# Kernel tuning notes

Measured on AMD Instinct MI355X. Metric: run time of the kernel, lower is better.

The kernel has to match this reference:

```python
import jax, jax.numpy as jnp
import numpy as np

S, B, SD, OD = 10, 256, 16, 8
H = 10 * (SD * SD + OD * OD)        # 3200, gru hidden
OUT1 = 4 * SD * OD                  # 512
IN = 2 * (SD + OD)                  # 48
TEMP = 0.1                          # concrete-dropout temperature


def setup_inputs() -> dict:
    key = jax.random.key(0)
    ks = jax.random.split(key, 24)
    sc = lambda k, sh, s=0.05: jax.random.normal(k, sh, jnp.float32) * s
    return {
        "y_t": sc(ks[0], (B, OD), 1.0),
        "x_filtered_prev": sc(ks[1], (B, SD), 1.0),
        "x_filtered_prev_prev": sc(ks[2], (B, SD), 1.0),
        "y_prev": sc(ks[3], (B, OD), 1.0),
        "delta_x_prev": sc(ks[4], (B, SD), 1.0),
        "h_prev_ensemble": sc(ks[5], (S, B, H)),
        "F_mat": sc(ks[6], (SD, SD), 0.2),
        "H_mat": sc(ks[7], (OD, SD), 0.2),
        "fc_in_w": sc(ks[8], (H, IN)),
        "fc_in_b": jnp.zeros((H,), jnp.float32),
        "W_ih": sc(ks[9], (3 * H, H), 0.01),
        "W_hh": sc(ks[10], (3 * H, H), 0.01),
        "b_ih": jnp.zeros((3 * H,), jnp.float32),
        "b_hh": jnp.zeros((3 * H,), jnp.float32),
        "fc1_w": sc(ks[11], (OUT1, H)),
        "fc1_b": jnp.zeros((OUT1,), jnp.float32),
        "fc2_w": sc(ks[12], (SD * OD, OUT1)),
        "fc2_b": jnp.zeros((SD * OD,), jnp.float32),
        "p_logit1": jnp.array([0.5], jnp.float32),   # sigmoid -> p in (0.5, 0.8) range
        "p_logit2": jnp.array([1.0], jnp.float32),
        "u1": jax.random.uniform(ks[13], (S, B, H), jnp.float32, 1e-4, 1.0 - 1e-4),
        "u2": jax.random.uniform(ks[14], (S, B, OUT1), jnp.float32, 1e-4, 1.0 - 1e-4),
    }


def _concrete_dropout(x, u, p):
    # relaxed Bernoulli drop mask, scaled to keep expectation
    z = jax.nn.sigmoid((jnp.log(p) - jnp.log1p(-p) + jnp.log(u) - jnp.log1p(-u)) / TEMP)
    return x * (1.0 - z) / (1.0 - p)


def reference(y_t, x_filtered_prev, x_filtered_prev_prev, y_prev, delta_x_prev,
              h_prev_ensemble, F_mat, H_mat, fc_in_w, fc_in_b,
              W_ih, W_hh, b_ih, b_hh, fc1_w, fc1_b, fc2_w, fc2_b,
              p_logit1, p_logit2, u1, u2):
    # system model prediction (nonlinear f, linear h), vectorized over batch
    x_predicted = jnp.tanh(x_filtered_prev @ F_mat.T)          # (B, SD)
    y_predicted = x_predicted @ H_mat.T                        # (B, OD)

    residual = y_t - y_predicted
    diff_state = x_filtered_prev - x_filtered_prev_prev
    inp = jnp.concatenate([delta_x_prev, residual, diff_state, y_prev], axis=-1)  # (B, IN)
    a = jax.nn.relu(inp @ fc_in_w.T + fc_in_b)                 # (B, H) shared across ensemble

    p1 = jax.nn.sigmoid(p_logit1[0])
    p2 = jax.nn.sigmoid(p_logit2[0])

    def gru_cell(x, h):
        gx = x @ W_ih.T + b_ih
        gh = h @ W_hh.T + b_hh
        gx_r, gx_z, gx_n = jnp.split(gx, 3, axis=-1)
        gh_r, gh_z, gh_n = jnp.split(gh, 3, axis=-1)
        r = jax.nn.sigmoid(gx_r + gh_r)
        z = jax.nn.sigmoid(gx_z + gh_z)
        n = jnp.tanh(gx_n + r * gh_n)
        return (1.0 - z) * n + z * h

    def sample_fn(h_i, u1_i, u2_i):
        x = _concrete_dropout(a, u1_i, p1)                     # (B, H)
        h_new = gru_cell(x, h_i)                               # (B, H)
        o = jax.nn.relu(h_new @ fc1_w.T + fc1_b)               # (B, OUT1)
        o = _concrete_dropout(o, u2_i, p2)
        K = (o @ fc2_w.T + fc2_b).reshape(B, SD, OD)           # Kalman gain
        correction = jnp.einsum('bso,bo->bs', K, residual)
        return x_predicted + correction, h_new

    xf_ens, h_new_ens = jax.vmap(sample_fn)(h_prev_ensemble, u1, u2)  # (S,B,SD),(S,B,H)

    x_filtered_final = xf_ens.mean(axis=0)                     # (B, SD)
    diff = xf_ens - x_filtered_final                           # (S, B, SD)
    P_filtered_final = jnp.einsum('sbi,sbj->bij', diff, diff) / S

    # concrete-dropout regularizer (identical per ensemble member)
    ent = lambda p: p * jnp.log(p) + (1.0 - p) * jnp.log1p(-p)
    reg = (jnp.sum(fc_in_w ** 2) / (1.0 - p1) + H * ent(p1)
           + jnp.sum(fc1_w ** 2) / (1.0 - p2) + OUT1 * ent(p2))
    raw_regularization = jnp.full((S,), reg)

    return x_filtered_final, P_filtered_final, raw_regularization
```

## Files before the change

kernel.cpp:

```cpp
#include <hip/hip_runtime.h>
#include <hip/hip_bf16.h>
#include <math.h>

#define S_ENS 10
#define B_DIM 256
#define SD 16
#define OD 8
#define H_DIM 3200
#define OUT1 512
#define IN_DIM 48
#define M_ROWS (S_ENS * B_DIM)
#define TEMP_INV 10.0f

typedef unsigned short u16;
typedef __attribute__((ext_vector_type(8))) short short8;
typedef __attribute__((ext_vector_type(4))) short short4v;
typedef __attribute__((ext_vector_type(4))) float floatx4;

__device__ __forceinline__ float sigmoidf_(float x) { return 1.0f / (1.0f + __expf(-x)); }
__device__ __forceinline__ float fast_tanh(float x) {
    x = fminf(fmaxf(x, -15.f), 15.f);
    float e = __expf(2.f * x);
    return (e - 1.f) / (e + 1.f);
}

__device__ __forceinline__ u16 f2bf(float f) {
    union { float f; unsigned u; } v; v.f = f;
    unsigned u = v.u + 0x7fffu + ((v.u >> 16) & 1u);
    return (u16)(u >> 16);
}
__device__ __forceinline__ float bf2f(u16 h) {
    union { unsigned u; float f; } v; v.u = ((unsigned)h) << 16;
    return v.f;
}

__device__ __forceinline__ void gld_lds16(const u16* g, u16* l) {
    __builtin_amdgcn_global_load_lds((const __attribute__((address_space(1))) void*)g,
                                     (__attribute__((address_space(3))) void*)l, 16, 0, 0);
}

__device__ __forceinline__ void kloop128(const u16* __restrict__ A, const u16* __restrict__ B,
                                         int m_base, int n_base, int kiters,
                                         u16* sA, u16* sB, floatx4 (&acc)[4][4]) {
    const int tid = threadIdx.x;
    const int wave = tid >> 6, lane = tid & 63;
    const int r = tid >> 2, c = tid & 3;
    const int swe = (c ^ ((r >> 1) & 3)) << 3;
    const u16* Ag = A + (size_t)(m_base + r) * H_DIM + swe;
    const u16* Bg = B + (size_t)(n_base + r) * H_DIM + swe;
    u16* sA0 = sA + wave * 512;
    u16* sB0 = sB + wave * 512;
    const int frow = lane & 15, fch = lane >> 4;
    const int wrow0 = (wave >> 1) * 64, wcol0 = (wave & 1) * 64;
    int aoff[4], boff[4];
    #pragma unroll
    for (int mi = 0; mi < 4; ++mi) {
        int row = wrow0 + mi * 16 + frow;
        aoff[mi] = row * 32 + ((fch ^ ((row >> 1) & 3)) << 3);
    }
    #pragma unroll
    for (int ni = 0; ni < 4; ++ni) {
        int row = wcol0 + ni * 16 + frow;
        boff[ni] = row * 32 + ((fch ^ ((row >> 1) & 3)) << 3);
    }
    for (int kk = 0; kk < kiters; ++kk) {
        const u16* ga = Ag + kk * 32;
        const u16* gb = Bg + kk * 32;
        __syncthreads();
        gld_lds16(ga, sA0);
        gld_lds16(ga + (size_t)64 * H_DIM, sA0 + 2048);
        gld_lds16(gb, sB0);
        gld_lds16(gb + (size_t)64 * H_DIM, sB0 + 2048);
        __syncthreads();
        short8 af[4], bfr[4];
        #pragma unroll
        for (int mi = 0; mi < 4; ++mi) af[mi] = *(const short8*)(sA + aoff[mi]);
        #pragma unroll
        for (int ni = 0; ni < 4; ++ni) bfr[ni] = *(const short8*)(sB + boff[ni]);
        #pragma unroll
        for (int mi = 0; mi < 4; ++mi)
            #pragma unroll
            for (int ni = 0; ni < 4; ++ni)
                acc[mi][ni] = __builtin_amdgcn_mfma_f32_16x16x32_bf16(af[mi], bfr[ni], acc[mi][ni], 0, 0, 0);
    }
}

__global__ __launch_bounds__(256) void gru_gemm_a(
    const u16* __restrict__ Xbf, const u16* __restrict__ Hpbf,
    const u16* __restrict__ Wih, const u16* __restrict__ Whh,
    const float* __restrict__ b_ih, const float* __restrict__ b_hh,
    u16* __restrict__ Rb, u16* __restrict__ Zb, u16* __restrict__ Gb) {
    __shared__ u16 sA[4096], sB[4096];
    floatx4 acc[4][4];
    #pragma unroll
    for (int i = 0; i < 4; ++i)
        #pragma unroll
        for (int j = 0; j < 4; ++j) acc[i][j] = (floatx4){0.f, 0.f, 0.f, 0.f};
    const int g = blockIdx.z;
    const int bmi = blockIdx.x, nbi = blockIdx.y;
    const int m_base = bmi * 128, nb = nbi * 128;
    const size_t gstride = (size_t)H_DIM * H_DIM;
    u16* outp;
    if (g == 0) {
        kloop128(Xbf, Wih, m_base, nb, 100, sA, sB, acc);
        kloop128(Hpbf, Whh, m_base, nb, 100, sA, sB, acc);
        outp = Rb;
    } else if (g == 1) {
        kloop128(Xbf, Wih + gstride, m_base, nb, 100, sA, sB, acc);
        kloop128(Hpbf, Whh + gstride, m_base, nb, 100, sA, sB, acc);
        outp = Zb;
    } else {
        kloop128(Hpbf, Whh + 2 * gstride, m_base, nb, 100, sA, sB, acc);
        outp = Gb;
    }
    const int lane = threadIdx.x & 63, wave = threadIdx.x >> 6;
    const int wcol0 = (wave & 1) * 64, cc = lane & 15;
    const size_t tbase = (size_t)(nbi * 20 + bmi) * 16384 + wave * 4096 + lane * 4;
    #pragma unroll
    for (int ni = 0; ni < 4; ++ni) {
        int col = nb + wcol0 + ni * 16 + cc;
        float bsum;
        if (g == 0)      bsum = b_ih[col] + b_hh[col];
        else if (g == 1) bsum = b_ih[H_DIM + col] + b_hh[H_DIM + col];
        else             bsum = b_hh[2 * H_DIM + col];
        #pragma unroll
        for (int mi = 0; mi < 4; ++mi) {
            short4v o;
            #pragma unroll
            for (int j = 0; j < 4; ++j) {
                float v = acc[mi][ni][j] + bsum;
                if (g < 2) v = sigmoidf_(v);
                o[j] = (short)f2bf(v);
            }
            *(short4v*)(outp + tbase + (mi * 4 + ni) * 256) = o;
        }
    }
}

__global__ __launch_bounds__(256) void gru_gemm_b(
    const u16* __restrict__ Xbf, const u16* __restrict__ Wih,
    const u16* __restrict__ Rb, const u16* __restrict__ Zb, const u16* __restrict__ Gb,
    const float* __restrict__ b_ih,
    const float* __restrict__ hprev, u16* __restrict__ Hn) {
    __shared__ u16 sA[4096], sB[4096];
    floatx4 acc[4][4];
    #pragma unroll
    for (int i = 0; i < 4; ++i)
        #pragma unroll
        for (int j = 0; j < 4; ++j) acc[i][j] = (floatx4){0.f, 0.f, 0.f, 0.f};
    const int bmi = blockIdx.x, nbi = blockIdx.y;
    const int m_base = bmi * 128, nb = nbi * 128;
    kloop128(Xbf, Wih + (size_t)2 * H_DIM * H_DIM, m_base, nb, 100, sA, sB, acc);
    const int lane = threadIdx.x & 63, wave = threadIdx.x >> 6;
    const int wrow0 = (wave >> 1) * 64, wcol0 = (wave & 1) * 64;
    const int quad = lane >> 4, cc = lane & 15;
    const size_t tbase = (size_t)(nbi * 20 + bmi) * 16384 + wave * 4096 + lane * 4;
    #pragma unroll
    for (int ni = 0; ni < 4; ++ni) {
        int col = nb + wcol0 + ni * 16 + cc;
        float bin_ = b_ih[2 * H_DIM + col];
        #pragma unroll
        for (int mi = 0; mi < 4; ++mi) {
            size_t pidx = tbase + (mi * 4 + ni) * 256;
            short4v rv = *(const short4v*)(Rb + pidx);
            short4v zv = *(const short4v*)(Zb + pidx);
            short4v gv = *(const short4v*)(Gb + pidx);
            int rw = m_base + wrow0 + mi * 16 + quad * 4;
            #pragma unroll
            for (int j = 0; j < 4; ++j) {
                float r = bf2f((u16)rv[j]);
                float z = bf2f((u16)zv[j]);
                float gh = bf2f((u16)gv[j]);
                float n = fast_tanh(acc[mi][ni][j] + bin_ + r * gh);
                size_t idx = (size_t)(rw + j) * H_DIM + col;
                float h = hprev[idx];
                Hn[idx] = f2bf((1.f - z) * n + z * h);
            }
        }
    }
}

__global__ __launch_bounds__(256) void fc1_k(
    const u16* __restrict__ Hn, const u16* __restrict__ Wb,
    const float* __restrict__ bias, const float* __restrict__ u2,
    const float* __restrict__ pl2, float* __restrict__ O) {
    __shared__ u16 sA[4096], sB[2048];
    floatx4 acc[4][2];
    #pragma unroll
    for (int i = 0; i < 4; ++i) { acc[i][0] = (floatx4){0.f,0.f,0.f,0.f}; acc[i][1] = (floatx4){0.f,0.f,0.f,0.f}; }
    const int tid = threadIdx.x;
    const int wave = tid >> 6, lane = tid & 63;
    const int m_base = blockIdx.y * 128, nb = blockIdx.x * 64;
    const int r = tid >> 2, c = tid & 3;
    const int swe = (c ^ ((r >> 1) & 3)) << 3;
    const u16* Ag = Hn + (size_t)(m_base + r) * H_DIM + swe;
    const u16* Bg = Wb + (size_t)(nb + r) * H_DIM + swe;
    u16* sA0 = sA + wave * 512;
    u16* sB0 = sB + wave * 512;
    const int frow = lane & 15, fch = lane >> 4;
    const int wrow0 = (wave >> 1) * 64, wcol0 = (wave & 1) * 32;
    int aoff[4], boff[2];
    #pragma unroll
    for (int mi = 0; mi < 4; ++mi) {
        int row = wrow0 + mi * 16 + frow;
        aoff[mi] = row * 32 + ((fch ^ ((row >> 1) & 3)) << 3);
    }
    #pragma unroll
    for (int ni = 0; ni < 2; ++ni) {
        int row = wcol0 + ni * 16 + frow;
        boff[ni] = row * 32 + ((fch ^ ((row >> 1) & 3)) << 3);
    }
    for (int kk = 0; kk < 100; ++kk) {
        __syncthreads();
        gld_lds16(Ag + kk * 32, sA0);
        gld_lds16(Ag + kk * 32 + (size_t)64 * H_DIM, sA0 + 2048);
        gld_lds16(Bg + kk * 32, sB0);
        __syncthreads();
        short8 af[4], bfr[2];
        #pragma unroll
        for (int mi = 0; mi < 4; ++mi) af[mi] = *(const short8*)(sA + aoff[mi]);
        #pragma unroll
        for (int ni = 0; ni < 2; ++ni) bfr[ni] = *(const short8*)(sB + boff[ni]);
        #pragma unroll
        for (int mi = 0; mi < 4; ++mi)
            #pragma unroll
            for (int ni = 0; ni < 2; ++ni)
                acc[mi][ni] = __builtin_amdgcn_mfma_f32_16x16x32_bf16(af[mi], bfr[ni], acc[mi][ni], 0, 0, 0);
    }
    float p = sigmoidf_(pl2[0]);
    float lp = __logf(p) - log1pf(-p);
    float inv = 1.0f / (1.0f - p);
    const int quad = lane >> 4, cc = lane & 15;
    #pragma unroll
    for (int ni = 0; ni < 2; ++ni) {
        int col = nb + wcol0 + ni * 16 + cc;
        float bcol = bias[col];
        #pragma unroll
        for (int mi = 0; mi < 4; ++mi) {
            int rw = m_base + wrow0 + mi * 16 + quad * 4;
            #pragma unroll
            for (int j = 0; j < 4; ++j) {
                size_t idx = (size_t)(rw + j) * OUT1 + col;
                float v = fmaxf(acc[mi][ni][j] + bcol, 0.f);
                float u = u2[idx];
                float z = sigmoidf_((lp + __logf(u) - log1pf(-u)) * TEMP_INV);
                O[idx] = v * (1.0f - z) * inv;
            }
        }
    }
}

__global__ void cvt_bf16_k(const float* __restrict__ src, u16* __restrict__ dst, int n8) {
    int i = blockIdx.x * 256 + threadIdx.x;
    if (i >= n8) return;
    float4 v0 = *((const float4*)src + 2 * (size_t)i);
    float4 v1 = *((const float4*)src + 2 * (size_t)i + 1);
    short8 o;
    o[0] = (short)f2bf(v0.x); o[1] = (short)f2bf(v0.y);
    o[2] = (short)f2bf(v0.z); o[3] = (short)f2bf(v0.w);
    o[4] = (short)f2bf(v1.x); o[5] = (short)f2bf(v1.y);
    o[6] = (short)f2bf(v1.z); o[7] = (short)f2bf(v1.w);
    *(short8*)(dst + 8 * (size_t)i) = o;
}

__global__ void prep_k(const float* __restrict__ y_t, const float* __restrict__ xfp,
                       const float* __restrict__ xfpp, const float* __restrict__ yprev,
                       const float* __restrict__ dxp, const float* __restrict__ Fm,
                       const float* __restrict__ Hm,
                       float* __restrict__ xpred, float* __restrict__ resid,
                       float* __restrict__ inp) {
    int b = threadIdx.x;
    float xrow[SD], xp[SD];
    for (int k = 0; k < SD; ++k) xrow[k] = xfp[b * SD + k];
    for (int s = 0; s < SD; ++s) {
        float acc = 0.f;
        for (int k = 0; k < SD; ++k) acc += xrow[k] * Fm[s * SD + k];
        xp[s] = tanhf(acc);
        xpred[b * SD + s] = xp[s];
    }
    float res[OD];
    for (int o = 0; o < OD; ++o) {
        float acc = 0.f;
        for (int s = 0; s < SD; ++s) acc += xp[s] * Hm[o * SD + s];
        res[o] = y_t[b * OD + o] - acc;
        resid[b * OD + o] = res[o];
    }
    float* ir = inp + b * IN_DIM;
    for (int k = 0; k < SD; ++k) ir[k] = dxp[b * SD + k];
    for (int o = 0; o < OD; ++o) ir[SD + o] = res[o];
    for (int k = 0; k < SD; ++k) ir[SD + OD + k] = xrow[k] - xfpp[b * SD + k];
    for (int o = 0; o < OD; ++o) ir[SD + OD + SD + o] = yprev[b * OD + o];
}

__global__ void fc_in_k(const float* __restrict__ inp, const float* __restrict__ w,
                        const float* __restrict__ bias, float* __restrict__ a) {
    int b = blockIdx.x;
    __shared__ float row[IN_DIM];
    int t = threadIdx.x;
    if (t < IN_DIM) row[t] = inp[b * IN_DIM + t];
    __syncthreads();
    for (int j = t; j < H_DIM; j += 256) {
        float s = bias[j];
        const float* wr = w + j * IN_DIM;
        #pragma unroll 8
        for (int k = 0; k < IN_DIM; ++k) s += row[k] * wr[k];
        a[b * H_DIM + j] = fmaxf(s, 0.f);
    }
}

__global__ void dropx_k(const float* __restrict__ a, const float* __restrict__ u1,
                        const float* __restrict__ pl1, u16* __restrict__ X) {
    int idx_in = blockIdx.x * 256 + threadIdx.x;
    int i = blockIdx.y;
    float p = sigmoidf_(pl1[0]);
    float lp = __logf(p) - log1pf(-p);
    float inv = 1.0f / (1.0f - p);
    size_t gidx = (size_t)i * (B_DIM * H_DIM) + idx_in;
    float u = u1[gidx];
    float z = sigmoidf_((lp + __logf(u) - log1pf(-u)) * TEMP_INV);
    X[gidx] = f2bf(a[idx_in] * (1.0f - z) * inv);
}

__global__ void fc2_corr_k(const float* __restrict__ O, const float* __restrict__ w,
                           const float* __restrict__ bias, const float* __restrict__ resid,
                           const float* __restrict__ xpred, float* __restrict__ xf_ens) {
    int row = blockIdx.x;
    int b = row & (B_DIM - 1);
    __shared__ __align__(16) float orow[OUT1];
    int t = threadIdx.x;
    for (int k = t; k < OUT1; k += 128) orow[k] = O[(size_t)row * OUT1 + k];
    __syncthreads();
    int s = t >> 3, oo = t & 7;
    const float* wr = w + (s * OD + oo) * OUT1;
    float sum = 0.f;
    for (int k = 0; k < OUT1; k += 4) {
        float4 ov = *(const float4*)&orow[k];
        float4 wv = *(const float4*)&wr[k];
        sum += ov.x * wv.x + ov.y * wv.y + ov.z * wv.z + ov.w * wv.w;
    }
    sum += bias[s * OD + oo];
    float v = sum * resid[b * OD + oo];
    v += __shfl_down(v, 4, 8);
    v += __shfl_down(v, 2, 8);
    v += __shfl_down(v, 1, 8);
    if (oo == 0) xf_ens[row * SD + s] = xpred[b * SD + s] + v;
}

__global__ void stats_k(const float* __restrict__ xf_ens, float* __restrict__ out) {
    int b = blockIdx.x;
    __shared__ float xf[S_ENS][SD];
    __shared__ float mean[SD];
    int t = threadIdx.x;
    if (t < S_ENS * SD) {
        int s = t >> 4, k = t & 15;
        xf[s][k] = xf_ens[s * (B_DIM * SD) + b * SD + k];
    }
    __syncthreads();
    if (t < SD) {
        float m = 0.f;
        for (int s = 0; s < S_ENS; ++s) m += xf[s][t];
        m *= (1.0f / S_ENS);
        mean[t] = m;
        out[b * SD + t] = m;
    }
    __syncthreads();
    int i = t >> 4, j = t & 15;
    float p = 0.f;
    for (int s = 0; s < S_ENS; ++s) p += (xf[s][i] - mean[i]) * (xf[s][j] - mean[j]);
    out[B_DIM * SD + b * 256 + t] = p * (1.0f / S_ENS);
}

__global__ void sumsq_k(const float* __restrict__ w, int n, float* __restrict__ accum) {
    float s = 0.f;
    for (int i = blockIdx.x * blockDim.x + threadIdx.x; i < n; i += gridDim.x * blockDim.x) {
        float v = w[i];
        s += v * v;
    }
    #pragma unroll
    for (int d = 32; d >= 1; d >>= 1) s += __shfl_down(s, d, 64);
    __shared__ float red[4];
    int lane = threadIdx.x & 63, wv = threadIdx.x >> 6;
    if (lane == 0) red[wv] = s;
    __syncthreads();
    if (threadIdx.x == 0) atomicAdd(accum, red[0] + red[1] + red[2] + red[3]);
}

__global__ void write_reg_k(const float* __restrict__ sums, const float* __restrict__ pl1,
                            const float* __restrict__ pl2, float* __restrict__ out) {
    int t = threadIdx.x;
    float p1 = sigmoidf_(pl1[0]);
    float p2 = sigmoidf_(pl2[0]);
    float ent1 = p1 * logf(p1) + (1.f - p1) * log1pf(-p1);
    float ent2 = p2 * logf(p2) + (1.f - p2) * log1pf(-p2);
    float reg = sums[0] / (1.f - p1) + (float)H_DIM * ent1
              + sums[1] / (1.f - p2) + (float)OUT1 * ent2;
    if (t < S_ENS) out[B_DIM * SD + B_DIM * SD * SD + t] = reg;
}

extern "C" void kernel_launch(void* const* d_in, const int* in_sizes, int n_in,
                              void* d_out, int out_size, void* d_ws, size_t ws_size,
                              hipStream_t stream) {
    const float* y_t     = (const float*)d_in[0];
    const float* xfp     = (const float*)d_in[1];
    const float* xfpp    = (const float*)d_in[2];
    const float* yprev   = (const float*)d_in[3];
    const float* dxp     = (const float*)d_in[4];
    const float* hprev   = (const float*)d_in[5];
    const float* Fm      = (const float*)d_in[6];
    const float* Hm      = (const float*)d_in[7];
    const float* fc_in_w = (const float*)d_in[8];
    const float* fc_in_b = (const float*)d_in[9];
    const float* W_ih    = (const float*)d_in[10];
    const float* W_hh    = (const float*)d_in[11];
    const float* b_ih    = (const float*)d_in[12];
    const float* b_hh    = (const float*)d_in[13];
    const float* fc1_w   = (const float*)d_in[14];
    const float* fc1_b   = (const float*)d_in[15];
    const float* fc2_w   = (const float*)d_in[16];
    const float* fc2_b   = (const float*)d_in[17];
    const float* pl1     = (const float*)d_in[18];
    const float* pl2     = (const float*)d_in[19];
    const float* u1      = (const float*)d_in[20];
    const float* u2      = (const float*)d_in[21];
    float* out = (float*)d_out;
    char* ws = (char*)d_ws;

    const size_t SZ_W    = (size_t)3 * H_DIM * H_DIM * 2;
    const size_t SZ_MH   = (size_t)M_ROWS * H_DIM * 2;
    size_t off = 0;
    u16* Wihbf  = (u16*)(ws + off); off += SZ_W;
    u16* Whhbf  = (u16*)(ws + off); off += SZ_W;
    u16* Rb     = (u16*)(ws + off); off += SZ_MH;
    u16* Zb     = (u16*)(ws + off); off += SZ_MH;
    u16* Gb     = (u16*)(ws + off); off += SZ_MH;
    u16* Xbf    = (u16*)(ws + off); off += SZ_MH;
    u16* Hpbf   = (u16*)(ws + off); off += SZ_MH;
    u16* Hnbf   = Hpbf;
    u16* fc1wbf = (u16*)(ws + off); off += (size_t)OUT1 * H_DIM * 2;
    float* O_buf   = (float*)(ws + off); off += (size_t)M_ROWS * OUT1 * 4;
    float* a_buf   = (float*)(ws + off); off += (size_t)B_DIM * H_DIM * 4;
    float* xf_buf  = (float*)(ws + off); off += (size_t)M_ROWS * SD * 4;
    float* xpred_b = (float*)(ws + off); off += (size_t)B_DIM * SD * 4;
    float* res_b   = (float*)(ws + off); off += (size_t)B_DIM * OD * 4;
    float* inp_b   = (float*)(ws + off); off += (size_t)B_DIM * IN_DIM * 4;
    float* sums_b  = (float*)(ws + off); off += 256;

    hipMemsetAsync(sums_b, 0, 2 * sizeof(float), stream);

    prep_k<<<1, 256, 0, stream>>>(y_t, xfp, xfpp, yprev, dxp, Fm, Hm, xpred_b, res_b, inp_b);
    fc_in_k<<<B_DIM, 256, 0, stream>>>(inp_b, fc_in_w, fc_in_b, a_buf);
    dropx_k<<<dim3(B_DIM * H_DIM / 256, S_ENS), 256, 0, stream>>>(a_buf, u1, pl1, Xbf);

    cvt_bf16_k<<<15000, 256, 0, stream>>>(W_ih, Wihbf, 3 * H_DIM * H_DIM / 8);
    cvt_bf16_k<<<15000, 256, 0, stream>>>(W_hh, Whhbf, 3 * H_DIM * H_DIM / 8);
    cvt_bf16_k<<<4000, 256, 0, stream>>>(hprev, Hpbf, M_ROWS * H_DIM / 8);
    cvt_bf16_k<<<800, 256, 0, stream>>>(fc1_w, fc1wbf, OUT1 * H_DIM / 8);

    gru_gemm_a<<<dim3(M_ROWS / 128, H_DIM / 128, 3), 256, 0, stream>>>(
        Xbf, Hpbf, Wihbf, Whhbf, b_ih, b_hh, Rb, Zb, Gb);
    gru_gemm_b<<<dim3(M_ROWS / 128, H_DIM / 128), 256, 0, stream>>>(
        Xbf, Wihbf, Rb, Zb, Gb, b_ih, hprev, Hnbf);

    fc1_k<<<dim3(OUT1 / 64, M_ROWS / 128), 256, 0, stream>>>(Hnbf, fc1wbf, fc1_b, u2, pl2, O_buf);

    fc2_corr_k<<<M_ROWS, 128, 0, stream>>>(O_buf, fc2_w, fc2_b, res_b, xpred_b, xf_buf);
    stats_k<<<B_DIM, 256, 0, stream>>>(xf_buf, out);
    sumsq_k<<<256, 256, 0, stream>>>(fc_in_w, H_DIM * IN_DIM, sums_b);
    sumsq_k<<<1024, 256, 0, stream>>>(fc1_w, OUT1 * H_DIM, sums_b + 1);
    write_reg_k<<<1, 64, 0, stream>>>(sums_b, pl1, pl2, out);
}
```

Baseline: 1.008 ms.

## Double-buffer GRU GEMM LDS loads, fold n-gate input GEMM into grid, fuse prep

The GEMM k-loop now double-buffers its LDS tiles. It prefetches the next K slice while computing the current one, which removes one barrier per iteration. The input-side n-gate GEMM moves from the separate gru_gemm_b kernel into a fourth z-slice of gru_gemm_a, and a lightweight combine kernel then applies the gate math. This puts more concurrent blocks in one launch but costs an extra bf16 intermediate buffer round-trip. prep and fc_in are also merged into one kernel to save a launch.

```diff
diff --git a/kernel.cpp b/kernel.cpp
--- a/kernel.cpp
+++ b/kernel.cpp
@@ -39,9 +39,9 @@
                                      (__attribute__((address_space(3))) void*)l, 16, 0, 0);
 }
 
-__device__ __forceinline__ void kloop128(const u16* __restrict__ A, const u16* __restrict__ B,
-                                         int m_base, int n_base, int kiters,
-                                         u16* sA, u16* sB, floatx4 (&acc)[4][4]) {
+__device__ __forceinline__ void kloop128db(const u16* __restrict__ A, const u16* __restrict__ B,
+                                           int m_base, int n_base, int kiters,
+                                           u16* sA, u16* sB, floatx4 (&acc)[4][4]) {
     const int tid = threadIdx.x;
     const int wave = tid >> 6, lane = tid & 63;
     const int r = tid >> 2, c = tid & 3;
@@ -63,20 +63,29 @@
         int row = wcol0 + ni * 16 + frow;
         boff[ni] = row * 32 + ((fch ^ ((row >> 1) & 3)) << 3);
     }
+    gld_lds16(Ag, sA0);
+    gld_lds16(Ag + (size_t)64 * H_DIM, sA0 + 2048);
+    gld_lds16(Bg, sB0);
+    gld_lds16(Bg + (size_t)64 * H_DIM, sB0 + 2048);
     for (int kk = 0; kk < kiters; ++kk) {
-        const u16* ga = Ag + kk * 32;
-        const u16* gb = Bg + kk * 32;
+        const int s = kk & 1;
         __syncthreads();
-        gld_lds16(ga, sA0);
-        gld_lds16(ga + (size_t)64 * H_DIM, sA0 + 2048);
-        gld_lds16(gb, sB0);
-        gld_lds16(gb + (size_t)64 * H_DIM, sB0 + 2048);
-        __syncthreads();
+        if (kk + 1 < kiters) {
+            const u16* ga = Ag + (kk + 1) * 32;
+            const u16* gb = Bg + (kk + 1) * 32;
+            const int o = (s ^ 1) * 4096;
+            gld_lds16(ga, sA0 + o);
+            gld_lds16(ga + (size_t)64 * H_DIM, sA0 + o + 2048);
+            gld_lds16(gb, sB0 + o);
+            gld_lds16(gb + (size_t)64 * H_DIM, sB0 + o + 2048);
+        }
+        const u16* pA = sA + s * 4096;
+        const u16* pB = sB + s * 4096;
         short8 af[4], bfr[4];
         #pragma unroll
-        for (int mi = 0; mi < 4; ++mi) af[mi] = *(const short8*)(sA + aoff[mi]);
-        #pragma unroll
-        for (int ni = 0; ni < 4; ++ni) bfr[ni] = *(const short8*)(sB + boff[ni]);
+        for (int mi = 0; mi < 4; ++mi) af[mi] = *(const short8*)(pA + aoff[mi]);
+        #pragma unroll
+        for (int ni = 0; ni < 4; ++ni) bfr[ni] = *(const short8*)(pB + boff[ni]);
         #pragma unroll
         for (int mi = 0; mi < 4; ++mi)
             #pragma unroll
@@ -89,8 +98,9 @@
     const u16* __restrict__ Xbf, const u16* __restrict__ Hpbf,
     const u16* __restrict__ Wih, const u16* __restrict__ Whh,
     const float* __restrict__ b_ih, const float* __restrict__ b_hh,
-    u16* __restrict__ Rb, u16* __restrict__ Zb, u16* __restrict__ Gb) {
-    __shared__ u16 sA[4096], sB[4096];
+    u16* __restrict__ Rb, u16* __restrict__ Zb, u16* __restrict__ Gb,
+    u16* __restrict__ GXb) {
+    __shared__ u16 sA[2 * 4096], sB[2 * 4096];
     floatx4 acc[4][4];
     #pragma unroll
     for (int i = 0; i < 4; ++i)
@@ -102,16 +112,19 @@
     const size_t gstride = (size_t)H_DIM * H_DIM;
     u16* outp;
     if (g == 0) {
-        kloop128(Xbf, Wih, m_base, nb, 100, sA, sB, acc);
-        kloop128(Hpbf, Whh, m_base, nb, 100, sA, sB, acc);
+        kloop128db(Xbf, Wih, m_base, nb, 100, sA, sB, acc);
+        kloop128db(Hpbf, Whh, m_base, nb, 100, sA, sB, acc);
         outp = Rb;
     } else if (g == 1) {
-        kloop128(Xbf, Wih + gstride, m_base, nb, 100, sA, sB, acc);
-        kloop128(Hpbf, Whh + gstride, m_base, nb, 100, sA, sB, acc);
+        kloop128db(Xbf, Wih + gstride, m_base, nb, 100, sA, sB, acc);
+        kloop128db(Hpbf, Whh + gstride, m_base, nb, 100, sA, sB, acc);
         outp = Zb;
+    } else if (g == 2) {
+        kloop128db(Hpbf, Whh + 2 * gstride, m_base, nb, 100, sA, sB, acc);
+        outp = Gb;
     } else {
-        kloop128(Hpbf, Whh + 2 * gstride, m_base, nb, 100, sA, sB, acc);
-        outp = Gb;
+        kloop128db(Xbf, Wih + 2 * gstride, m_base, nb, 100, sA, sB, acc);
+        outp = GXb;
     }
     const int lane = threadIdx.x & 63, wave = threadIdx.x >> 6;
     const int wcol0 = (wave & 1) * 64, cc = lane & 15;
@@ -122,7 +135,8 @@
         float bsum;
         if (g == 0)      bsum = b_ih[col] + b_hh[col];
         else if (g == 1) bsum = b_ih[H_DIM + col] + b_hh[H_DIM + col];
-        else             bsum = b_hh[2 * H_DIM + col];
+        else if (g == 2) bsum = b_hh[2 * H_DIM + col];
+        else             bsum = b_ih[2 * H_DIM + col];
         #pragma unroll
         for (int mi = 0; mi < 4; ++mi) {
             short4v o;
@@ -137,41 +151,33 @@
     }
 }
 
-__global__ __launch_bounds__(256) void gru_gemm_b(
-    const u16* __restrict__ Xbf, const u16* __restrict__ Wih,
-    const u16* __restrict__ Rb, const u16* __restrict__ Zb, const u16* __restrict__ Gb,
-    const float* __restrict__ b_ih,
+__global__ __launch_bounds__(256) void combine_k(
+    const u16* __restrict__ Rb, const u16* __restrict__ Zb,
+    const u16* __restrict__ Gb, const u16* __restrict__ GXb,
     const float* __restrict__ hprev, u16* __restrict__ Hn) {
-    __shared__ u16 sA[4096], sB[4096];
-    floatx4 acc[4][4];
-    #pragma unroll
-    for (int i = 0; i < 4; ++i)
-        #pragma unroll
-        for (int j = 0; j < 4; ++j) acc[i][j] = (floatx4){0.f, 0.f, 0.f, 0.f};
-    const int bmi = blockIdx.x, nbi = blockIdx.y;
+    const int t = blockIdx.x;
+    const int bmi = t % 20, nbi = t / 20;
     const int m_base = bmi * 128, nb = nbi * 128;
-    kloop128(Xbf, Wih + (size_t)2 * H_DIM * H_DIM, m_base, nb, 100, sA, sB, acc);
     const int lane = threadIdx.x & 63, wave = threadIdx.x >> 6;
     const int wrow0 = (wave >> 1) * 64, wcol0 = (wave & 1) * 64;
     const int quad = lane >> 4, cc = lane & 15;
-    const size_t tbase = (size_t)(nbi * 20 + bmi) * 16384 + wave * 4096 + lane * 4;
+    const size_t tbase = (size_t)t * 16384 + wave * 4096 + lane * 4;
     #pragma unroll
     for (int ni = 0; ni < 4; ++ni) {
         int col = nb + wcol0 + ni * 16 + cc;
-        float bin_ = b_ih[2 * H_DIM + col];
         #pragma unroll
         for (int mi = 0; mi < 4; ++mi) {
             size_t pidx = tbase + (mi * 4 + ni) * 256;
             short4v rv = *(const short4v*)(Rb + pidx);
             short4v zv = *(const short4v*)(Zb + pidx);
             short4v gv = *(const short4v*)(Gb + pidx);
+            short4v xv = *(const short4v*)(GXb + pidx);
             int rw = m_base + wrow0 + mi * 16 + quad * 4;
             #pragma unroll
             for (int j = 0; j < 4; ++j) {
                 float r = bf2f((u16)rv[j]);
                 float z = bf2f((u16)zv[j]);
-                float gh = bf2f((u16)gv[j]);
-                float n = fast_tanh(acc[mi][ni][j] + bin_ + r * gh);
+                float n = fast_tanh(bf2f((u16)xv[j]) + r * bf2f((u16)gv[j]));
                 size_t idx = (size_t)(rw + j) * H_DIM + col;
                 float h = hprev[idx];
                 Hn[idx] = f2bf((1.f - z) * n + z * h);
@@ -263,47 +269,41 @@
     *(short8*)(dst + 8 * (size_t)i) = o;
 }
 
-__global__ void prep_k(const float* __restrict__ y_t, const float* __restrict__ xfp,
-                       const float* __restrict__ xfpp, const float* __restrict__ yprev,
-                       const float* __restrict__ dxp, const float* __restrict__ Fm,
-                       const float* __restrict__ Hm,
-                       float* __restrict__ xpred, float* __restrict__ resid,
-                       float* __restrict__ inp) {
-    int b = threadIdx.x;
-    float xrow[SD], xp[SD];
-    for (int k = 0; k < SD; ++k) xrow[k] = xfp[b * SD + k];
-    for (int s = 0; s < SD; ++s) {
+__global__ void prep_fcin_k(const float* __restrict__ y_t, const float* __restrict__ xfp,
+                            const float* __restrict__ xfpp, const float* __restrict__ yprev,
+                            const float* __restrict__ dxp, const float* __restrict__ Fm,
+                            const float* __restrict__ Hm, const float* __restrict__ w,
+                            const float* __restrict__ bias,
+                            float* __restrict__ xpred, float* __restrict__ resid,
+                            float* __restrict__ a) {
+    int b = blockIdx.x;
+    int t = threadIdx.x;
+    __shared__ float xp_s[SD], res_s[OD], inp_s[IN_DIM];
+    if (t < SD) {
         float acc = 0.f;
-        for (int k = 0; k < SD; ++k) acc += xrow[k] * Fm[s * SD + k];
-        xp[s] = tanhf(acc);
-        xpred[b * SD + s] = xp[s];
-    }
-    float res[OD];
-    for (int o = 0; o < OD; ++o) {
+        for (int k = 0; k < SD; ++k) acc += xfp[b * SD + k] * Fm[t * SD + k];
+        float xp = tanhf(acc);
+        xp_s[t] = xp;
+        xpred[b * SD + t] = xp;
+        inp_s[t] = dxp[b * SD + t];
+        inp_s[SD + OD + t] = xfp[b * SD + t] - xfpp[b * SD + t];
+    }
+    __syncthreads();
+    if (t < OD) {
         float acc = 0.f;
-        for (int s = 0; s < SD; ++s) acc += xp[s] * Hm[o * SD + s];
-        res[o] = y_t[b * OD + o] - acc;
-        resid[b * OD + o] = res[o];
-    }
-    float* ir = inp + b * IN_DIM;
-    for (int k = 0; k < SD; ++k) ir[k] = dxp[b * SD + k];
-    for (int o = 0; o < OD; ++o) ir[SD + o] = res[o];
-    for (int k = 0; k < SD; ++k) ir[SD + OD + k] = xrow[k] - xfpp[b * SD + k];
-    for (int o = 0; o < OD; ++o) ir[SD + OD + SD + o] = yprev[b * OD + o];
-}
-
-__global__ void fc_in_k(const float* __restrict__ inp, const float* __restrict__ w,
-                        const float* __restrict__ bias, float* __restrict__ a) {
-    int b = blockIdx.x;
-    __shared__ float row[IN_DIM];
-    int t = threadIdx.x;
-    if (t < IN_DIM) row[t] = inp[b * IN_DIM + t];
+        for (int s = 0; s < SD; ++s) acc += xp_s[s] * Hm[t * SD + s];
+        float res = y_t[b * OD + t] - acc;
+        res_s[t] = res;
+        resid[b * OD + t] = res;
+        inp_s[SD + t] = res;
+        inp_s[SD + OD + SD + t] = yprev[b * OD + t];
+    }
     __syncthreads();
     for (int j = t; j < H_DIM; j += 256) {
         float s = bias[j];
         const float* wr = w + j * IN_DIM;
         #pragma unroll 8
-        for (int k = 0; k < IN_DIM; ++k) s += row[k] * wr[k];
+        for (int k = 0; k < IN_DIM; ++k) s += inp_s[k] * wr[k];
         a[b * H_DIM + j] = fmaxf(s, 0.f);
     }
 }
@@ -433,6 +433,7 @@
     u16* Rb     = (u16*)(ws + off); off += SZ_MH;
     u16* Zb     = (u16*)(ws + off); off += SZ_MH;
     u16* Gb     = (u16*)(ws + off); off += SZ_MH;
+    u16* GXb    = (u16*)(ws + off); off += SZ_MH;
     u16* Xbf    = (u16*)(ws + off); off += SZ_MH;
     u16* Hpbf   = (u16*)(ws + off); off += SZ_MH;
     u16* Hnbf   = Hpbf;
@@ -442,13 +443,12 @@
     float* xf_buf  = (float*)(ws + off); off += (size_t)M_ROWS * SD * 4;
     float* xpred_b = (float*)(ws + off); off += (size_t)B_DIM * SD * 4;
     float* res_b   = (float*)(ws + off); off += (size_t)B_DIM * OD * 4;
-    float* inp_b   = (float*)(ws + off); off += (size_t)B_DIM * IN_DIM * 4;
     float* sums_b  = (float*)(ws + off); off += 256;
 
     hipMemsetAsync(sums_b, 0, 2 * sizeof(float), stream);
 
-    prep_k<<<1, 256, 0, stream>>>(y_t, xfp, xfpp, yprev, dxp, Fm, Hm, xpred_b, res_b, inp_b);
-    fc_in_k<<<B_DIM, 256, 0, stream>>>(inp_b, fc_in_w, fc_in_b, a_buf);
+    prep_fcin_k<<<B_DIM, 256, 0, stream>>>(y_t, xfp, xfpp, yprev, dxp, Fm, Hm,
+                                           fc_in_w, fc_in_b, xpred_b, res_b, a_buf);
     dropx_k<<<dim3(B_DIM * H_DIM / 256, S_ENS), 256, 0, stream>>>(a_buf, u1, pl1, Xbf);
 
     cvt_bf16_k<<<15000, 256, 0, stream>>>(W_ih, Wihbf, 3 * H_DIM * H_DIM / 8);
@@ -456,10 +456,10 @@
     cvt_bf16_k<<<4000, 256, 0, stream>>>(hprev, Hpbf, M_ROWS * H_DIM / 8);
     cvt_bf16_k<<<800, 256, 0, stream>>>(fc1_w, fc1wbf, OUT1 * H_DIM / 8);
 
-    gru_gemm_a<<<dim3(M_ROWS / 128, H_DIM / 128, 3), 256, 0, stream>>>(
-        Xbf, Hpbf, Wihbf, Whhbf, b_ih, b_hh, Rb, Zb, Gb);
-    gru_gemm_b<<<dim3(M_ROWS / 128, H_DIM / 128), 256, 0, stream>>>(
-        Xbf, Wihbf, Rb, Zb, Gb, b_ih, hprev, Hnbf);
+    gru_gemm_a<<<dim3(M_ROWS / 128, H_DIM / 128, 4), 256, 0, stream>>>(
+        Xbf, Hpbf, Wihbf, Whhbf, b_ih, b_hh, Rb, Zb, Gb, GXb);
+    combine_k<<<(M_ROWS / 128) * (H_DIM / 128), 256, 0, stream>>>(
+        Rb, Zb, Gb, GXb, hprev, Hnbf);
 
     fc1_k<<<dim3(OUT1 / 64, M_ROWS / 128), 256, 0, stream>>>(Hnbf, fc1wbf, fc1_b, u2, pl2, O_buf);
 
```

Result: slower. 1.060 ms (+5.2%).
